# Kernel tuning notes

Hardware: AMD Instinct MI355X
Metric: run time of the kernel (lower is better)

The kernel has to match this reference:

```python
import jax, jax.numpy as jnp
import numpy as np

B, S, HID = 4, 1024, 1024
H = 16
D = HID // H  # 64
SPARSITY = 0.9  # keep prob = 0.1


def setup_inputs() -> dict:
    key = jax.random.key(0)
    ks = jax.random.split(key, 11)
    sc = 1.0 / np.sqrt(HID)
    x = jax.random.normal(ks[0], (B, S, HID), dtype=jnp.float32)
    Wq = jax.random.normal(ks[1], (HID, HID), dtype=jnp.float32) * sc
    bq = jnp.zeros((HID,), dtype=jnp.float32)
    Wk = jax.random.normal(ks[2], (HID, HID), dtype=jnp.float32) * sc
    bk = jnp.zeros((HID,), dtype=jnp.float32)
    Wv = jax.random.normal(ks[3], (HID, HID), dtype=jnp.float32) * sc
    bv = jnp.zeros((HID,), dtype=jnp.float32)
    Wo = jax.random.normal(ks[4], (HID, HID), dtype=jnp.float32) * sc
    bo = jnp.zeros((HID,), dtype=jnp.float32)
    temperature = jnp.ones((H, 1, 1), dtype=jnp.float32)
    # training-mode random sparsity mask: rand > sparsity -> keep (True)
    sparse_mask = jax.random.uniform(ks[5], (B, H, S, S)) > SPARSITY
    return {"x": x, "Wq": Wq, "bq": bq, "Wk": Wk, "bk": bk, "Wv": Wv,
            "bv": bv, "Wo": Wo, "bo": bo, "temperature": temperature,
            "sparse_mask": sparse_mask}


def reference(x, Wq, bq, Wk, bk, Wv, bv, Wo, bo, temperature, sparse_mask):
    b, s, _ = x.shape
    def split_heads(t):
        return t.reshape(b, s, H, D).transpose(0, 2, 1, 3)  # [B,H,S,D]
    q = split_heads(x @ Wq + bq)
    k = split_heads(x @ Wk + bk)
    v = split_heads(x @ Wv + bv)
    scores = jnp.einsum('bhqd,bhkd->bhqk', q, k) / np.sqrt(D)
    scores = scores * temperature  # [H,1,1] broadcasts over [B,H,S,S]
    scores = jnp.where(sparse_mask, scores, -jnp.inf)
    attn = jax.nn.softmax(scores, axis=-1)
    out = jnp.einsum('bhqk,bhkd->bhqd', attn, v)
    out = out.transpose(0, 2, 1, 3).reshape(b, s, HID)
    return out @ Wo + bo
```

## Files before the change

### kernel.cpp

```cpp
#include <hip/hip_runtime.h>

typedef unsigned short u16;
typedef short short8 __attribute__((ext_vector_type(8)));
typedef float f32x4 __attribute__((ext_vector_type(4)));
typedef float float4v __attribute__((ext_vector_type(4)));
typedef u16 u16x4 __attribute__((ext_vector_type(4)));
typedef unsigned long long u64;

__device__ __forceinline__ u16 f2bf(float f) {
  union { float f; unsigned u; } v; v.f = f;
  unsigned r = v.u + 0x7FFFu + ((v.u >> 16) & 1u);
  return (u16)(r >> 16);
}

__device__ __forceinline__ unsigned cvtpk(float lo, float hi) {
  unsigned r;
  asm("v_cvt_pk_bf16_f32 %0, %1, %2" : "=v"(r) : "v"(lo), "v"(hi));
  return r;
}

__device__ __forceinline__ void gload16(const u16* g, u16* l) {
  __builtin_amdgcn_global_load_lds(
      (const __attribute__((address_space(1))) void*)g,
      (__attribute__((address_space(3))) void*)l, 16, 0, 0);
}

__global__ __launch_bounds__(256)
void maskbits_kernel(const void* __restrict__ mask, u64* __restrict__ bits) {
  __shared__ int sf;
  if (threadIdx.x == 0) sf = 0;
  __syncthreads();
  {
    uint4 v = ((const uint4*)mask)[threadIdx.x];
    unsigned xs[4] = {v.x, v.y, v.z, v.w};
    int f = 0;
#pragma unroll
    for (int d = 0; d < 4; ++d) {
      unsigned u = xs[d];
      if (u == 0x3F800000u) f |= 1;
      if (u & 0xFFFFFF00u) f |= 2;
      if ((d & 1) && u) f |= 4;
    }
    if (f) atomicOr(&sf, f);
  }
  __syncthreads();
  const int fl = sf;
  const int fmt = (fl & 1) ? 2 : ((fl & 2) ? 0 : ((fl & 4) ? 1 : 3));

  const int wi = blockIdx.x * 256 + threadIdx.x;
  u64 b = 0;
  if (fmt == 0) {
    const uint4* mp = (const uint4*)mask + (size_t)wi * 4;
#pragma unroll
    for (int i = 0; i < 4; ++i) {
      uint4 v = mp[i];
      unsigned x[4] = {v.x, v.y, v.z, v.w};
#pragma unroll
      for (int d = 0; d < 4; ++d)
#pragma unroll
        for (int by = 0; by < 4; ++by)
          if (x[d] & (0xFFu << (by * 8))) b |= 1ULL << (i * 16 + d * 4 + by);
    }
  } else if (fmt != 3) {
    const uint4* mp = (const uint4*)mask + (size_t)wi * 16;
#pragma unroll
    for (int i = 0; i < 16; ++i) {
      uint4 v = mp[i];
      if (v.x) b |= 1ULL << (i * 4 + 0);
      if (v.y) b |= 1ULL << (i * 4 + 1);
      if (v.z) b |= 1ULL << (i * 4 + 2);
      if (v.w) b |= 1ULL << (i * 4 + 3);
    }
  } else {
    const uint4* mp = (const uint4*)mask + (size_t)wi * 32;
#pragma unroll
    for (int i = 0; i < 32; ++i) {
      uint4 v = mp[i];
      if (v.x | v.y) b |= 1ULL << (i * 2 + 0);
      if (v.z | v.w) b |= 1ULL << (i * 2 + 1);
    }
  }
  int bh = wi >> 14, q = (wi >> 4) & 1023, kt = wi & 15;
  bits[((size_t)bh * 16 + kt) * 1024 + q] = b;
}

__global__ __launch_bounds__(256) void xcvt_kernel(const float* __restrict__ x, u16* __restrict__ xb) {
  int i = (blockIdx.x * 256 + threadIdx.x) * 4;
  float4v v = *(const float4v*)(x + i);
  u16x4 o;
  o[0] = f2bf(v[0]); o[1] = f2bf(v[1]); o[2] = f2bf(v[2]); o[3] = f2bf(v[3]);
  *(u16x4*)(xb + i) = o;
}

__global__ __launch_bounds__(256) void wcvt_kernel(
    const float* __restrict__ W0, const float* __restrict__ W1,
    const float* __restrict__ W2, const float* __restrict__ W3,
    u16* __restrict__ Wt) {
  __shared__ float t[32][33];
  int z = blockIdx.z;
  const float* W = (z == 0) ? W0 : (z == 1) ? W1 : (z == 2) ? W2 : W3;
  u16* out = Wt + (size_t)z * 1024 * 1024;
  int n0 = blockIdx.x * 32, k0 = blockIdx.y * 32;
  int tx = threadIdx.x & 31, ty = threadIdx.x >> 5;
#pragma unroll
  for (int j = 0; j < 4; ++j)
    t[ty + 8 * j][tx] = W[(size_t)(k0 + ty + 8 * j) * 1024 + n0 + tx];
  __syncthreads();
#pragma unroll
  for (int j = 0; j < 4; ++j)
    out[(size_t)(n0 + ty + 8 * j) * 1024 + k0 + tx] = f2bf(t[tx][ty + 8 * j]);
}

__global__ __launch_bounds__(256)
void gemm128_kernel(const u16* __restrict__ A,
                    const u16* __restrict__ BtQ, const u16* __restrict__ BtK, const u16* __restrict__ BtV,
                    const float* __restrict__ bQ, const float* __restrict__ bK, const float* __restrict__ bV,
                    const float* __restrict__ temp,
                    u16* __restrict__ qb, u16* __restrict__ kb, u16* __restrict__ vT,
                    float* __restrict__ fo, int phase) {
  constexpr int K = 1024;
  __shared__ u16 As[128 * 32];
  __shared__ u16 Bs[128 * 32];
  const int tid = threadIdx.x;
  const int lane = tid & 63, w = tid >> 6;
  const int l15 = lane & 15, l4 = lane >> 4;
  const int m0 = blockIdx.x * 128, n0 = blockIdx.y * 128;
  const int z = blockIdx.z;
  const u16* Bt = (z == 0) ? BtQ : (z == 1) ? BtK : BtV;
  const float* bias = (z == 0) ? bQ : (z == 1) ? bK : bV;
  const int wr = w >> 1, wc = w & 1;

  f32x4 acc[4][4] = {};

  const int c0 = tid, c1 = 256 + tid;
  const u16* ga0 = A + (size_t)(m0 + (c0 >> 2)) * K + (c0 & 3) * 8;
  const u16* ga1 = A + (size_t)(m0 + (c1 >> 2)) * K + (c1 & 3) * 8;
  const u16* gb0 = Bt + (size_t)(n0 + (c0 >> 2)) * K + (c0 & 3) * 8;
  const u16* gb1 = Bt + (size_t)(n0 + (c1 >> 2)) * K + (c1 & 3) * 8;
  u16* la0 = As + c0 * 8;
  u16* la1 = As + c1 * 8;
  u16* lb0 = Bs + c0 * 8;
  u16* lb1 = Bs + c1 * 8;

  for (int kt = 0; kt < K; kt += 32) {
    gload16(ga0 + kt, la0);
    gload16(ga1 + kt, la1);
    gload16(gb0 + kt, lb0);
    gload16(gb1 + kt, lb1);
    __syncthreads();
    short8 af[4], bfr[4];
#pragma unroll
    for (int r = 0; r < 4; ++r)
      af[r] = *(const short8*)(As + (wr * 64 + r * 16 + l15) * 32 + l4 * 8);
#pragma unroll
    for (int c = 0; c < 4; ++c)
      bfr[c] = *(const short8*)(Bs + (wc * 64 + c * 16 + l15) * 32 + l4 * 8);
#pragma unroll
    for (int r = 0; r < 4; ++r)
#pragma unroll
      for (int c = 0; c < 4; ++c)
        acc[r][c] = __builtin_amdgcn_mfma_f32_16x16x32_bf16(af[r], bfr[c], acc[r][c], 0, 0, 0);
    __syncthreads();
  }

  float bv4[4], fac4[4];
#pragma unroll
  for (int c = 0; c < 4; ++c) {
    int col = n0 + wc * 64 + c * 16 + l15;
    bv4[c] = bias[col];
    fac4[c] = (phase == 0 && z == 0) ? temp[col >> 6] * 0.18033688011112042f : 1.0f;
  }

#pragma unroll
  for (int r = 0; r < 4; ++r) {
#pragma unroll
    for (int c = 0; c < 4; ++c) {
#pragma unroll
      for (int j = 0; j < 4; ++j) {
        float val = (acc[r][c][j] + bv4[c]) * fac4[c];
        int row = m0 + wr * 64 + r * 16 + l4 * 4 + j;
        int col = n0 + wc * 64 + c * 16 + l15;
        if (phase == 0) {
          int b = row >> 10, s = row & 1023, hh = col >> 6, d = col & 63;
          if (z < 2) {
            u16* dst = (z == 0) ? qb : kb;
            dst[(((size_t)b * 16 + hh) * 1024 + s) * 64 + d] = f2bf(val);
          } else {
            vT[(((size_t)b * 16 + hh) * 64 + d) * 1024 + s] = f2bf(val);
          }
        } else {
          fo[(size_t)row * 1024 + col] = val;
        }
      }
    }
  }
}

__device__ __forceinline__ void softmax_pwrite(const f32x4* s, u64 wcur,
                                               float& m, float& l, f32x4* oacc,
                                               char* Prow, int swzP, int l4) {
  float xx[4][4];
#pragma unroll
  for (int cb = 0; cb < 4; ++cb) {
    unsigned nib = (unsigned)(wcur >> (cb * 16 + l4 * 4)) & 15u;
#pragma unroll
    for (int j = 0; j < 4; ++j)
      xx[cb][j] = ((nib >> j) & 1) ? s[cb][j] : -1e30f;
  }
  float mt = xx[0][0];
#pragma unroll
  for (int cb = 0; cb < 4; ++cb)
#pragma unroll
    for (int j = 0; j < 4; ++j) mt = fmaxf(mt, xx[cb][j]);
  mt = fmaxf(mt, __shfl_xor(mt, 16));
  mt = fmaxf(mt, __shfl_xor(mt, 32));
  if (!__all(mt <= m + 8.f)) {
    float mnew = fmaxf(m, mt);
    float al = exp2f(m - mnew);
    l *= al;
#pragma unroll
    for (int db = 0; db < 4; ++db) oacc[db] *= al;
    m = mnew;
  }
  float rs = 0.f;
#pragma unroll
  for (int cb = 0; cb < 4; ++cb)
#pragma unroll
    for (int j = 0; j < 4; ++j) {
      xx[cb][j] = exp2f(xx[cb][j] - m);
      rs += xx[cb][j];
    }
  rs += __shfl_xor(rs, 16);
  rs += __shfl_xor(rs, 32);
  l += rs;
#pragma unroll
  for (int cb = 0; cb < 4; ++cb) {
    unsigned w0 = cvtpk(xx[cb][0], xx[cb][1]);
    unsigned w1 = cvtpk(xx[cb][2], xx[cb][3]);
    unsigned o2[2] = {w0, w1};
    *(unsigned long long*)(Prow + ((cb * 32 + l4 * 8) ^ swzP)) = *(unsigned long long*)o2;
  }
}

__global__ __launch_bounds__(256)
void attn_kernel(const u16* __restrict__ qb, const u16* __restrict__ kb, const u16* __restrict__ vT,
                 const u64* __restrict__ mbits, u16* __restrict__ oh) {
  __shared__ u16 Ks[2][64 * 64];
  __shared__ u16 Vs[2][64 * 64];
  __shared__ u16 P[4][32 * 64];
  const int tid = threadIdx.x, lane = tid & 63, w = tid >> 6;
  const int l15 = lane & 15, l4 = lane >> 4;
  const int id = blockIdx.x;
  const int xcd = id & 7, sl = id >> 3;
  const int bh = xcd * 8 + (sl >> 3), qx = sl & 7;
  const int b = bh >> 4, h = bh & 15;
  const int q0 = qx * 128 + w * 32;
  const u16* qp = qb + ((size_t)bh * 1024 + q0) * 64;
  const u16* kp = kb + (size_t)bh * 1024 * 64;
  const u16* vp = vT + (size_t)bh * 64 * 1024;
  char* Pw = (char*)&P[w][0];
  const int swzP = (l15 & 7) << 4;
  char* ProwA = Pw + l15 * 128;
  char* ProwB = Pw + (16 + l15) * 128;

  const int L0 = tid, L1 = tid + 256;
  const int r0 = L0 >> 3, cc0 = (L0 & 7) ^ (r0 & 7);
  const int r1 = L1 >> 3, cc1 = (L1 & 7) ^ (r1 & 7);
  const int swzK = (l15 & 7) << 3;

  short8 qa0 = *(const short8*)(qp + (size_t)l15 * 64 + l4 * 8);
  short8 qa1 = *(const short8*)(qp + (size_t)l15 * 64 + 32 + l4 * 8);
  short8 qb0 = *(const short8*)(qp + (size_t)(16 + l15) * 64 + l4 * 8);
  short8 qb1 = *(const short8*)(qp + (size_t)(16 + l15) * 64 + 32 + l4 * 8);

  float ma = -1e30f, la = 0.f, mb_ = -1e30f, lb = 0.f;
  f32x4 oa[4] = {}, ob[4] = {};

  const u64* mba = mbits + (size_t)bh * 16 * 1024 + q0 + l15;
  u64 wa = mba[0], wb = mba[16];

  gload16(kp + (size_t)r0 * 64 + cc0 * 8, &Ks[0][L0 * 8]);
  gload16(kp + (size_t)r1 * 64 + cc1 * 8, &Ks[0][L1 * 8]);
  gload16(vp + (size_t)r0 * 1024 + cc0 * 8, &Vs[0][L0 * 8]);
  gload16(vp + (size_t)r1 * 1024 + cc1 * 8, &Vs[0][L1 * 8]);

  for (int t = 0; t < 16; ++t) {
    const int buf = t & 1;
    __syncthreads();

    if (t < 15) {
      const int k1 = (t + 1) * 64;
      gload16(kp + (size_t)(k1 + r0) * 64 + cc0 * 8, &Ks[buf ^ 1][L0 * 8]);
      gload16(kp + (size_t)(k1 + r1) * 64 + cc1 * 8, &Ks[buf ^ 1][L1 * 8]);
      gload16(vp + (size_t)r0 * 1024 + k1 + cc0 * 8, &Vs[buf ^ 1][L0 * 8]);
      gload16(vp + (size_t)r1 * 1024 + k1 + cc1 * 8, &Vs[buf ^ 1][L1 * 8]);
    }
    u64 wan = 0, wbn = 0;
    if (t < 15) { wan = mba[(t + 1) * 1024]; wbn = mba[(t + 1) * 1024 + 16]; }

    f32x4 sa[4] = {}, sb[4] = {};
    __builtin_amdgcn_s_setprio(1);
#pragma unroll
    for (int cb = 0; cb < 4; ++cb) {
      const u16* kr = &Ks[buf][(cb * 16 + l15) * 64];
      short8 kf0 = *(const short8*)(kr + ((l4 * 8) ^ swzK));
      short8 kf1 = *(const short8*)(kr + ((32 + l4 * 8) ^ swzK));
      sa[cb] = __builtin_amdgcn_mfma_f32_16x16x32_bf16(kf0, qa0, sa[cb], 0, 0, 0);
      sa[cb] = __builtin_amdgcn_mfma_f32_16x16x32_bf16(kf1, qa1, sa[cb], 0, 0, 0);
      sb[cb] = __builtin_amdgcn_mfma_f32_16x16x32_bf16(kf0, qb0, sb[cb], 0, 0, 0);
      sb[cb] = __builtin_amdgcn_mfma_f32_16x16x32_bf16(kf1, qb1, sb[cb], 0, 0, 0);
    }
    __builtin_amdgcn_s_setprio(0);

    softmax_pwrite(sa, wa, ma, la, oa, ProwA, swzP, l4);
    softmax_pwrite(sb, wb, mb_, lb, ob, ProwB, swzP, l4);

    __builtin_amdgcn_s_setprio(1);
#pragma unroll
    for (int ks = 0; ks < 2; ++ks) {
      short8 pa = *(const short8*)(ProwA + ((ks * 64 + l4 * 16) ^ swzP));
      short8 pb = *(const short8*)(ProwB + ((ks * 64 + l4 * 16) ^ swzP));
#pragma unroll
      for (int db = 0; db < 4; ++db) {
        short8 vf = *(const short8*)(&Vs[buf][(db * 16 + l15) * 64 + ((ks * 32 + l4 * 8) ^ swzK)]);
        oa[db] = __builtin_amdgcn_mfma_f32_16x16x32_bf16(vf, pa, oa[db], 0, 0, 0);
        ob[db] = __builtin_amdgcn_mfma_f32_16x16x32_bf16(vf, pb, ob[db], 0, 0, 0);
      }
    }
    __builtin_amdgcn_s_setprio(0);
    wa = wan; wb = wbn;
  }

  float rla = 1.f / la, rlb = 1.f / lb;
  u16* orowA = oh + ((size_t)b * 1024 + q0 + l15) * 1024 + h * 64;
  u16* orowB = oh + ((size_t)b * 1024 + q0 + 16 + l15) * 1024 + h * 64;
#pragma unroll
  for (int db = 0; db < 4; ++db) {
    unsigned a0 = cvtpk(oa[db][0] * rla, oa[db][1] * rla);
    unsigned a1 = cvtpk(oa[db][2] * rla, oa[db][3] * rla);
    unsigned b0 = cvtpk(ob[db][0] * rlb, ob[db][1] * rlb);
    unsigned b1 = cvtpk(ob[db][2] * rlb, ob[db][3] * rlb);
    unsigned oA[2] = {a0, a1}, oB[2] = {b0, b1};
    *(unsigned long long*)(orowA + db * 16 + l4 * 4) = *(unsigned long long*)oA;
    *(unsigned long long*)(orowB + db * 16 + l4 * 4) = *(unsigned long long*)oB;
  }
}

extern "C" void kernel_launch(void* const* d_in, const int* in_sizes, int n_in,
                              void* d_out, int out_size, void* d_ws, size_t ws_size,
                              hipStream_t stream) {
  const float* x = (const float*)d_in[0];
  const float* Wq = (const float*)d_in[1];
  const float* bq = (const float*)d_in[2];
  const float* Wk = (const float*)d_in[3];
  const float* bk = (const float*)d_in[4];
  const float* Wv = (const float*)d_in[5];
  const float* bv = (const float*)d_in[6];
  const float* Wo = (const float*)d_in[7];
  const float* bo = (const float*)d_in[8];
  const float* temp = (const float*)d_in[9];
  const void* mask = (const void*)d_in[10];

  char* ws = (char*)d_ws;
  u16* xb = (u16*)(ws + 256);
  u16* Wt = xb + (size_t)4 * 1024 * 1024;
  u16* qbuf = Wt + (size_t)4 * 1024 * 1024;
  u16* kbuf = qbuf + (size_t)4 * 1024 * 1024;
  u16* vTb = kbuf + (size_t)4 * 1024 * 1024;
  u64* mbits = (u64*)(vTb + (size_t)4 * 1024 * 1024);
  u16* oh = xb;

  maskbits_kernel<<<4096, 256, 0, stream>>>(mask, mbits);
  xcvt_kernel<<<4096, 256, 0, stream>>>(x, xb);
  wcvt_kernel<<<dim3(32, 32, 4), 256, 0, stream>>>(Wq, Wk, Wv, Wo, Wt);
  gemm128_kernel<<<dim3(32, 8, 3), 256, 0, stream>>>(
      xb, Wt, Wt + 1024 * 1024, Wt + 2 * 1024 * 1024,
      bq, bk, bv, temp, qbuf, kbuf, vTb, nullptr, 0);
  attn_kernel<<<512, 256, 0, stream>>>(qbuf, kbuf, vTb, mbits, oh);
  gemm128_kernel<<<dim3(32, 8, 1), 256, 0, stream>>>(
      oh, Wt + 3 * 1024 * 1024, nullptr, nullptr,
      bo, nullptr, nullptr, temp, nullptr, nullptr, nullptr, (float*)d_out, 1);
}
```

Before: 193.1 us.

## Merge prep kernels, transpose V epilogue, widen attention KV tiles, narrow output GEMM

Merges the three preprocessing kernels (mask bit-packing, x conversion, weight transpose/convert) into one launch selected by block index. The V projection now swaps MFMA operands so the transposed V store is contiguous along the sequence. The attention loop loads 128 keys per stage, halving the number of barriers and iterations. The output GEMM uses a 64-wide N tile so it launches twice as many blocks. Together these aim to cut launch overhead, scattered stores and sync cost, at the price of more LDS per attention block and possibly lower occupancy.

```diff
diff --git a/kernel.cpp b/kernel.cpp
--- a/kernel.cpp
+++ b/kernel.cpp
@@ -26,111 +26,116 @@
 }
 
 __global__ __launch_bounds__(256)
-void maskbits_kernel(const void* __restrict__ mask, u64* __restrict__ bits) {
+void prep_kernel(const void* __restrict__ mask, u64* __restrict__ bits,
+                 const float* __restrict__ x, u16* __restrict__ xb,
+                 const float* __restrict__ W0, const float* __restrict__ W1,
+                 const float* __restrict__ W2, const float* __restrict__ W3,
+                 u16* __restrict__ Wt) {
+  __shared__ float t[32][33];
   __shared__ int sf;
-  if (threadIdx.x == 0) sf = 0;
-  __syncthreads();
-  {
-    uint4 v = ((const uint4*)mask)[threadIdx.x];
-    unsigned xs[4] = {v.x, v.y, v.z, v.w};
-    int f = 0;
-#pragma unroll
-    for (int d = 0; d < 4; ++d) {
-      unsigned u = xs[d];
-      if (u == 0x3F800000u) f |= 1;
-      if (u & 0xFFFFFF00u) f |= 2;
-      if ((d & 1) && u) f |= 4;
-    }
-    if (f) atomicOr(&sf, f);
-  }
-  __syncthreads();
-  const int fl = sf;
-  const int fmt = (fl & 1) ? 2 : ((fl & 2) ? 0 : ((fl & 4) ? 1 : 3));
-
-  const int wi = blockIdx.x * 256 + threadIdx.x;
-  u64 b = 0;
-  if (fmt == 0) {
-    const uint4* mp = (const uint4*)mask + (size_t)wi * 4;
-#pragma unroll
-    for (int i = 0; i < 4; ++i) {
-      uint4 v = mp[i];
-      unsigned x[4] = {v.x, v.y, v.z, v.w};
-#pragma unroll
-      for (int d = 0; d < 4; ++d)
-#pragma unroll
-        for (int by = 0; by < 4; ++by)
-          if (x[d] & (0xFFu << (by * 8))) b |= 1ULL << (i * 16 + d * 4 + by);
-    }
-  } else if (fmt != 3) {
-    const uint4* mp = (const uint4*)mask + (size_t)wi * 16;
-#pragma unroll
-    for (int i = 0; i < 16; ++i) {
-      uint4 v = mp[i];
-      if (v.x) b |= 1ULL << (i * 4 + 0);
-      if (v.y) b |= 1ULL << (i * 4 + 1);
-      if (v.z) b |= 1ULL << (i * 4 + 2);
-      if (v.w) b |= 1ULL << (i * 4 + 3);
-    }
+  const int bid = blockIdx.x;
+  if (bid < 4096) {
+    if (threadIdx.x == 0) sf = 0;
+    __syncthreads();
+    {
+      uint4 v = ((const uint4*)mask)[threadIdx.x];
+      unsigned xs[4] = {v.x, v.y, v.z, v.w};
+      int f = 0;
+#pragma unroll
+      for (int d = 0; d < 4; ++d) {
+        unsigned u = xs[d];
+        if (u == 0x3F800000u) f |= 1;
+        if (u & 0xFFFFFF00u) f |= 2;
+        if ((d & 1) && u) f |= 4;
+      }
+      if (f) atomicOr(&sf, f);
+    }
+    __syncthreads();
+    const int fl = sf;
+    const int fmt = (fl & 1) ? 2 : ((fl & 2) ? 0 : ((fl & 4) ? 1 : 3));
+
+    const int wi = bid * 256 + threadIdx.x;
+    u64 b = 0;
+    if (fmt == 0) {
+      const uint4* mp = (const uint4*)mask + (size_t)wi * 4;
+#pragma unroll
+      for (int i = 0; i < 4; ++i) {
+        uint4 v = mp[i];
+        unsigned xw[4] = {v.x, v.y, v.z, v.w};
+#pragma unroll
+        for (int d = 0; d < 4; ++d)
+#pragma unroll
+          for (int by = 0; by < 4; ++by)
+            if (xw[d] & (0xFFu << (by * 8))) b |= 1ULL << (i * 16 + d * 4 + by);
+      }
+    } else if (fmt != 3) {
+      const uint4* mp = (const uint4*)mask + (size_t)wi * 16;
+#pragma unroll
+      for (int i = 0; i < 16; ++i) {
+        uint4 v = mp[i];
+        if (v.x) b |= 1ULL << (i * 4 + 0);
+        if (v.y) b |= 1ULL << (i * 4 + 1);
+        if (v.z) b |= 1ULL << (i * 4 + 2);
+        if (v.w) b |= 1ULL << (i * 4 + 3);
+      }
+    } else {
+      const uint4* mp = (const uint4*)mask + (size_t)wi * 32;
+#pragma unroll
+      for (int i = 0; i < 32; ++i) {
+        uint4 v = mp[i];
+        if (v.x | v.y) b |= 1ULL << (i * 2 + 0);
+        if (v.z | v.w) b |= 1ULL << (i * 2 + 1);
+      }
+    }
+    int bh = wi >> 14, q = (wi >> 4) & 1023, kt = wi & 15;
+    bits[((size_t)bh * 16 + kt) * 1024 + q] = b;
+  } else if (bid < 8192) {
+    int i = ((bid - 4096) * 256 + threadIdx.x) * 4;
+    float4v v = *(const float4v*)(x + i);
+    u16x4 o;
+    o[0] = f2bf(v[0]); o[1] = f2bf(v[1]); o[2] = f2bf(v[2]); o[3] = f2bf(v[3]);
+    *(u16x4*)(xb + i) = o;
   } else {
-    const uint4* mp = (const uint4*)mask + (size_t)wi * 32;
-#pragma unroll
-    for (int i = 0; i < 32; ++i) {
-      uint4 v = mp[i];
-      if (v.x | v.y) b |= 1ULL << (i * 2 + 0);
-      if (v.z | v.w) b |= 1ULL << (i * 2 + 1);
-    }
-  }
-  int bh = wi >> 14, q = (wi >> 4) & 1023, kt = wi & 15;
-  bits[((size_t)bh * 16 + kt) * 1024 + q] = b;
-}
-
-__global__ __launch_bounds__(256) void xcvt_kernel(const float* __restrict__ x, u16* __restrict__ xb) {
-  int i = (blockIdx.x * 256 + threadIdx.x) * 4;
-  float4v v = *(const float4v*)(x + i);
-  u16x4 o;
-  o[0] = f2bf(v[0]); o[1] = f2bf(v[1]); o[2] = f2bf(v[2]); o[3] = f2bf(v[3]);
-  *(u16x4*)(xb + i) = o;
-}
-
-__global__ __launch_bounds__(256) void wcvt_kernel(
-    const float* __restrict__ W0, const float* __restrict__ W1,
-    const float* __restrict__ W2, const float* __restrict__ W3,
-    u16* __restrict__ Wt) {
-  __shared__ float t[32][33];
-  int z = blockIdx.z;
-  const float* W = (z == 0) ? W0 : (z == 1) ? W1 : (z == 2) ? W2 : W3;
-  u16* out = Wt + (size_t)z * 1024 * 1024;
-  int n0 = blockIdx.x * 32, k0 = blockIdx.y * 32;
-  int tx = threadIdx.x & 31, ty = threadIdx.x >> 5;
-#pragma unroll
-  for (int j = 0; j < 4; ++j)
-    t[ty + 8 * j][tx] = W[(size_t)(k0 + ty + 8 * j) * 1024 + n0 + tx];
-  __syncthreads();
-#pragma unroll
-  for (int j = 0; j < 4; ++j)
-    out[(size_t)(n0 + ty + 8 * j) * 1024 + k0 + tx] = f2bf(t[tx][ty + 8 * j]);
-}
-
+    int i = bid - 8192;
+    int z = i >> 10, rest = i & 1023;
+    const float* W = (z == 0) ? W0 : (z == 1) ? W1 : (z == 2) ? W2 : W3;
+    u16* out = Wt + (size_t)z * 1024 * 1024;
+    int n0 = (rest & 31) * 32, k0 = (rest >> 5) * 32;
+    int tx = threadIdx.x & 31, ty = threadIdx.x >> 5;
+#pragma unroll
+    for (int j = 0; j < 4; ++j)
+      t[ty + 8 * j][tx] = W[(size_t)(k0 + ty + 8 * j) * 1024 + n0 + tx];
+    __syncthreads();
+#pragma unroll
+    for (int j = 0; j < 4; ++j)
+      out[(size_t)(n0 + ty + 8 * j) * 1024 + k0 + tx] = f2bf(t[tx][ty + 8 * j]);
+  }
+}
+
+template<int BN>
 __global__ __launch_bounds__(256)
-void gemm128_kernel(const u16* __restrict__ A,
-                    const u16* __restrict__ BtQ, const u16* __restrict__ BtK, const u16* __restrict__ BtV,
-                    const float* __restrict__ bQ, const float* __restrict__ bK, const float* __restrict__ bV,
-                    const float* __restrict__ temp,
-                    u16* __restrict__ qb, u16* __restrict__ kb, u16* __restrict__ vT,
-                    float* __restrict__ fo, int phase) {
+void gemm_kernel(const u16* __restrict__ A,
+                 const u16* __restrict__ Bt0, const u16* __restrict__ Bt1, const u16* __restrict__ Bt2,
+                 const float* __restrict__ b0, const float* __restrict__ b1, const float* __restrict__ b2,
+                 const float* __restrict__ temp,
+                 u16* __restrict__ qb, u16* __restrict__ kb, u16* __restrict__ vT,
+                 float* __restrict__ fo, int phase) {
   constexpr int K = 1024;
+  constexpr int WN = BN / 2;
+  constexpr int NC = WN / 16;
   __shared__ u16 As[128 * 32];
-  __shared__ u16 Bs[128 * 32];
+  __shared__ u16 Bs[BN * 32];
   const int tid = threadIdx.x;
   const int lane = tid & 63, w = tid >> 6;
   const int l15 = lane & 15, l4 = lane >> 4;
-  const int m0 = blockIdx.x * 128, n0 = blockIdx.y * 128;
+  const int m0 = blockIdx.x * 128, n0 = blockIdx.y * BN;
   const int z = blockIdx.z;
-  const u16* Bt = (z == 0) ? BtQ : (z == 1) ? BtK : BtV;
-  const float* bias = (z == 0) ? bQ : (z == 1) ? bK : bV;
+  const u16* Bt = (z == 0) ? Bt0 : (z == 1) ? Bt1 : Bt2;
+  const float* bias = (z == 0) ? b0 : (z == 1) ? b1 : b2;
   const int wr = w >> 1, wc = w & 1;
-
-  f32x4 acc[4][4] = {};
+  const bool ct = (phase == 0) && (z == 2);
+
+  f32x4 acc[4][NC] = {};
 
   const int c0 = tid, c1 = 256 + tid;
   const u16* ga0 = A + (size_t)(m0 + (c0 >> 2)) * K + (c0 & 3) * 8;
@@ -146,50 +151,76 @@
     gload16(ga0 + kt, la0);
     gload16(ga1 + kt, la1);
     gload16(gb0 + kt, lb0);
-    gload16(gb1 + kt, lb1);
-    __syncthreads();
-    short8 af[4], bfr[4];
+    if (BN == 128) gload16(gb1 + kt, lb1);
+    __syncthreads();
+    short8 af[4], bfr[NC];
 #pragma unroll
     for (int r = 0; r < 4; ++r)
       af[r] = *(const short8*)(As + (wr * 64 + r * 16 + l15) * 32 + l4 * 8);
 #pragma unroll
-    for (int c = 0; c < 4; ++c)
-      bfr[c] = *(const short8*)(Bs + (wc * 64 + c * 16 + l15) * 32 + l4 * 8);
-#pragma unroll
-    for (int r = 0; r < 4; ++r)
-#pragma unroll
-      for (int c = 0; c < 4; ++c)
-        acc[r][c] = __builtin_amdgcn_mfma_f32_16x16x32_bf16(af[r], bfr[c], acc[r][c], 0, 0, 0);
-    __syncthreads();
-  }
-
-  float bv4[4], fac4[4];
-#pragma unroll
-  for (int c = 0; c < 4; ++c) {
-    int col = n0 + wc * 64 + c * 16 + l15;
-    bv4[c] = bias[col];
-    fac4[c] = (phase == 0 && z == 0) ? temp[col >> 6] * 0.18033688011112042f : 1.0f;
-  }
-
-#pragma unroll
-  for (int r = 0; r < 4; ++r) {
-#pragma unroll
-    for (int c = 0; c < 4; ++c) {
-#pragma unroll
-      for (int j = 0; j < 4; ++j) {
-        float val = (acc[r][c][j] + bv4[c]) * fac4[c];
-        int row = m0 + wr * 64 + r * 16 + l4 * 4 + j;
-        int col = n0 + wc * 64 + c * 16 + l15;
-        if (phase == 0) {
-          int b = row >> 10, s = row & 1023, hh = col >> 6, d = col & 63;
-          if (z < 2) {
+    for (int c = 0; c < NC; ++c)
+      bfr[c] = *(const short8*)(Bs + (wc * WN + c * 16 + l15) * 32 + l4 * 8);
+    if (ct) {
+#pragma unroll
+      for (int r = 0; r < 4; ++r)
+#pragma unroll
+        for (int c = 0; c < NC; ++c)
+          acc[r][c] = __builtin_amdgcn_mfma_f32_16x16x32_bf16(bfr[c], af[r], acc[r][c], 0, 0, 0);
+    } else {
+#pragma unroll
+      for (int r = 0; r < 4; ++r)
+#pragma unroll
+        for (int c = 0; c < NC; ++c)
+          acc[r][c] = __builtin_amdgcn_mfma_f32_16x16x32_bf16(af[r], bfr[c], acc[r][c], 0, 0, 0);
+    }
+    __syncthreads();
+  }
+
+  if (ct) {
+    float bvj[NC][4];
+#pragma unroll
+    for (int c = 0; c < NC; ++c)
+#pragma unroll
+      for (int j = 0; j < 4; ++j)
+        bvj[c][j] = bias[n0 + wc * WN + c * 16 + l4 * 4 + j];
+#pragma unroll
+    for (int r = 0; r < 4; ++r) {
+#pragma unroll
+      for (int c = 0; c < NC; ++c) {
+#pragma unroll
+        for (int j = 0; j < 4; ++j) {
+          float val = acc[r][c][j] + bvj[c][j];
+          int n = n0 + wc * WN + c * 16 + l4 * 4 + j;
+          int mm = m0 + wr * 64 + r * 16 + l15;
+          int b = mm >> 10, s = mm & 1023;
+          vT[((size_t)b * 1024 + n) * 1024 + s] = f2bf(val);
+        }
+      }
+    }
+  } else {
+    float bv4[NC], fac4[NC];
+#pragma unroll
+    for (int c = 0; c < NC; ++c) {
+      int col = n0 + wc * WN + c * 16 + l15;
+      bv4[c] = bias[col];
+      fac4[c] = (phase == 0 && z == 0) ? temp[col >> 6] * 0.18033688011112042f : 1.0f;
+    }
+#pragma unroll
+    for (int r = 0; r < 4; ++r) {
+#pragma unroll
+      for (int c = 0; c < NC; ++c) {
+#pragma unroll
+        for (int j = 0; j < 4; ++j) {
+          float val = (acc[r][c][j] + bv4[c]) * fac4[c];
+          int row = m0 + wr * 64 + r * 16 + l4 * 4 + j;
+          int col = n0 + wc * WN + c * 16 + l15;
+          if (phase == 0) {
+            int b = row >> 10, s = row & 1023, hh = col >> 6, d = col & 63;
             u16* dst = (z == 0) ? qb : kb;
             dst[(((size_t)b * 16 + hh) * 1024 + s) * 64 + d] = f2bf(val);
           } else {
-            vT[(((size_t)b * 16 + hh) * 64 + d) * 1024 + s] = f2bf(val);
+            fo[(size_t)row * 1024 + col] = val;
           }
-        } else {
-          fo[(size_t)row * 1024 + col] = val;
         }
       }
     }
@@ -245,8 +276,8 @@
 __global__ __launch_bounds__(256)
 void attn_kernel(const u16* __restrict__ qb, const u16* __restrict__ kb, const u16* __restrict__ vT,
                  const u64* __restrict__ mbits, u16* __restrict__ oh) {
-  __shared__ u16 Ks[2][64 * 64];
-  __shared__ u16 Vs[2][64 * 64];
+  __shared__ u16 Ks[2][128 * 64];
+  __shared__ u16 Vs[2][64 * 128];
   __shared__ u16 P[4][32 * 64];
   const int tid = threadIdx.x, lane = tid & 63, w = tid >> 6;
   const int l15 = lane & 15, l4 = lane >> 4;
@@ -262,73 +293,88 @@
   const int swzP = (l15 & 7) << 4;
   char* ProwA = Pw + l15 * 128;
   char* ProwB = Pw + (16 + l15) * 128;
-
-  const int L0 = tid, L1 = tid + 256;
-  const int r0 = L0 >> 3, cc0 = (L0 & 7) ^ (r0 & 7);
-  const int r1 = L1 >> 3, cc1 = (L1 & 7) ^ (r1 & 7);
   const int swzK = (l15 & 7) << 3;
+
+  int krow[4], kcol[4], vrow[4], vcol[4];
+#pragma unroll
+  for (int i = 0; i < 4; ++i) {
+    int c = tid + 256 * i;
+    krow[i] = c >> 3; kcol[i] = ((c & 7) ^ (krow[i] & 7)) * 8;
+    vrow[i] = c >> 4; vcol[i] = ((c & 15) ^ (vrow[i] & 7)) * 8;
+  }
 
   short8 qa0 = *(const short8*)(qp + (size_t)l15 * 64 + l4 * 8);
   short8 qa1 = *(const short8*)(qp + (size_t)l15 * 64 + 32 + l4 * 8);
   short8 qb0 = *(const short8*)(qp + (size_t)(16 + l15) * 64 + l4 * 8);
   short8 qb1 = *(const short8*)(qp + (size_t)(16 + l15) * 64 + 32 + l4 * 8);
 
-  float ma = -1e30f, la = 0.f, mb_ = -1e30f, lb = 0.f;
+  float ma = -1e30f, la = 0.f, mbv = -1e30f, lb = 0.f;
   f32x4 oa[4] = {}, ob[4] = {};
 
   const u64* mba = mbits + (size_t)bh * 16 * 1024 + q0 + l15;
-  u64 wa = mba[0], wb = mba[16];
-
-  gload16(kp + (size_t)r0 * 64 + cc0 * 8, &Ks[0][L0 * 8]);
-  gload16(kp + (size_t)r1 * 64 + cc1 * 8, &Ks[0][L1 * 8]);
-  gload16(vp + (size_t)r0 * 1024 + cc0 * 8, &Vs[0][L0 * 8]);
-  gload16(vp + (size_t)r1 * 1024 + cc1 * 8, &Vs[0][L1 * 8]);
-
-  for (int t = 0; t < 16; ++t) {
+  u64 wa[2], wb[2];
+  wa[0] = mba[0]; wa[1] = mba[1024];
+  wb[0] = mba[16]; wb[1] = mba[1024 + 16];
+
+#pragma unroll
+  for (int i = 0; i < 4; ++i) {
+    gload16(kp + (size_t)krow[i] * 64 + kcol[i], &Ks[0][(tid + 256 * i) * 8]);
+    gload16(vp + (size_t)vrow[i] * 1024 + vcol[i], &Vs[0][(tid + 256 * i) * 8]);
+  }
+
+  for (int t = 0; t < 8; ++t) {
     const int buf = t & 1;
     __syncthreads();
 
-    if (t < 15) {
-      const int k1 = (t + 1) * 64;
-      gload16(kp + (size_t)(k1 + r0) * 64 + cc0 * 8, &Ks[buf ^ 1][L0 * 8]);
-      gload16(kp + (size_t)(k1 + r1) * 64 + cc1 * 8, &Ks[buf ^ 1][L1 * 8]);
-      gload16(vp + (size_t)r0 * 1024 + k1 + cc0 * 8, &Vs[buf ^ 1][L0 * 8]);
-      gload16(vp + (size_t)r1 * 1024 + k1 + cc1 * 8, &Vs[buf ^ 1][L1 * 8]);
-    }
-    u64 wan = 0, wbn = 0;
-    if (t < 15) { wan = mba[(t + 1) * 1024]; wbn = mba[(t + 1) * 1024 + 16]; }
-
-    f32x4 sa[4] = {}, sb[4] = {};
-    __builtin_amdgcn_s_setprio(1);
-#pragma unroll
-    for (int cb = 0; cb < 4; ++cb) {
-      const u16* kr = &Ks[buf][(cb * 16 + l15) * 64];
-      short8 kf0 = *(const short8*)(kr + ((l4 * 8) ^ swzK));
-      short8 kf1 = *(const short8*)(kr + ((32 + l4 * 8) ^ swzK));
-      sa[cb] = __builtin_amdgcn_mfma_f32_16x16x32_bf16(kf0, qa0, sa[cb], 0, 0, 0);
-      sa[cb] = __builtin_amdgcn_mfma_f32_16x16x32_bf16(kf1, qa1, sa[cb], 0, 0, 0);
-      sb[cb] = __builtin_amdgcn_mfma_f32_16x16x32_bf16(kf0, qb0, sb[cb], 0, 0, 0);
-      sb[cb] = __builtin_amdgcn_mfma_f32_16x16x32_bf16(kf1, qb1, sb[cb], 0, 0, 0);
-    }
-    __builtin_amdgcn_s_setprio(0);
-
-    softmax_pwrite(sa, wa, ma, la, oa, ProwA, swzP, l4);
-    softmax_pwrite(sb, wb, mb_, lb, ob, ProwB, swzP, l4);
-
-    __builtin_amdgcn_s_setprio(1);
-#pragma unroll
-    for (int ks = 0; ks < 2; ++ks) {
-      short8 pa = *(const short8*)(ProwA + ((ks * 64 + l4 * 16) ^ swzP));
-      short8 pb = *(const short8*)(ProwB + ((ks * 64 + l4 * 16) ^ swzP));
-#pragma unroll
-      for (int db = 0; db < 4; ++db) {
-        short8 vf = *(const short8*)(&Vs[buf][(db * 16 + l15) * 64 + ((ks * 32 + l4 * 8) ^ swzK)]);
-        oa[db] = __builtin_amdgcn_mfma_f32_16x16x32_bf16(vf, pa, oa[db], 0, 0, 0);
-        ob[db] = __builtin_amdgcn_mfma_f32_16x16x32_bf16(vf, pb, ob[db], 0, 0, 0);
-      }
-    }
-    __builtin_amdgcn_s_setprio(0);
-    wa = wan; wb = wbn;
+    if (t < 7) {
+      const int k1 = (t + 1) * 128;
+#pragma unroll
+      for (int i = 0; i < 4; ++i) {
+        gload16(kp + (size_t)(k1 + krow[i]) * 64 + kcol[i], &Ks[buf ^ 1][(tid + 256 * i) * 8]);
+        gload16(vp + (size_t)vrow[i] * 1024 + k1 + vcol[i], &Vs[buf ^ 1][(tid + 256 * i) * 8]);
+      }
+    }
+    u64 nwa[2] = {0, 0}, nwb[2] = {0, 0};
+    if (t < 7) {
+      nwa[0] = mba[(2 * t + 2) * 1024];      nwa[1] = mba[(2 * t + 3) * 1024];
+      nwb[0] = mba[(2 * t + 2) * 1024 + 16]; nwb[1] = mba[(2 * t + 3) * 1024 + 16];
+    }
+
+#pragma unroll
+    for (int st = 0; st < 2; ++st) {
+      f32x4 sa[4] = {}, sb[4] = {};
+      __builtin_amdgcn_s_setprio(1);
+#pragma unroll
+      for (int cb = 0; cb < 4; ++cb) {
+        const u16* kr = &Ks[buf][(st * 64 + cb * 16 + l15) * 64];
+        short8 kf0 = *(const short8*)(kr + ((l4 * 8) ^ swzK));
+        short8 kf1 = *(const short8*)(kr + ((32 + l4 * 8) ^ swzK));
+        sa[cb] = __builtin_amdgcn_mfma_f32_16x16x32_bf16(kf0, qa0, sa[cb], 0, 0, 0);
+        sa[cb] = __builtin_amdgcn_mfma_f32_16x16x32_bf16(kf1, qa1, sa[cb], 0, 0, 0);
+        sb[cb] = __builtin_amdgcn_mfma_f32_16x16x32_bf16(kf0, qb0, sb[cb], 0, 0, 0);
+        sb[cb] = __builtin_amdgcn_mfma_f32_16x16x32_bf16(kf1, qb1, sb[cb], 0, 0, 0);
+      }
+      __builtin_amdgcn_s_setprio(0);
+
+      softmax_pwrite(sa, wa[st], ma, la, oa, ProwA, swzP, l4);
+      softmax_pwrite(sb, wb[st], mbv, lb, ob, ProwB, swzP, l4);
+
+      __builtin_amdgcn_s_setprio(1);
+#pragma unroll
+      for (int ks = 0; ks < 2; ++ks) {
+        short8 pa = *(const short8*)(ProwA + ((ks * 64 + l4 * 16) ^ swzP));
+        short8 pbf = *(const short8*)(ProwB + ((ks * 64 + l4 * 16) ^ swzP));
+#pragma unroll
+        for (int db = 0; db < 4; ++db) {
+          short8 vf = *(const short8*)(&Vs[buf][(db * 16 + l15) * 128 +
+                                                ((st * 64 + ks * 32 + l4 * 8) ^ swzK)]);
+          oa[db] = __builtin_amdgcn_mfma_f32_16x16x32_bf16(vf, pa, oa[db], 0, 0, 0);
+          ob[db] = __builtin_amdgcn_mfma_f32_16x16x32_bf16(vf, pbf, ob[db], 0, 0, 0);
+        }
+      }
+      __builtin_amdgcn_s_setprio(0);
+    }
+    wa[0] = nwa[0]; wa[1] = nwa[1]; wb[0] = nwb[0]; wb[1] = nwb[1];
   }
 
   float rla = 1.f / la, rlb = 1.f / lb;
@@ -370,14 +416,12 @@
   u64* mbits = (u64*)(vTb + (size_t)4 * 1024 * 1024);
   u16* oh = xb;
 
-  maskbits_kernel<<<4096, 256, 0, stream>>>(mask, mbits);
-  xcvt_kernel<<<4096, 256, 0, stream>>>(x, xb);
-  wcvt_kernel<<<dim3(32, 32, 4), 256, 0, stream>>>(Wq, Wk, Wv, Wo, Wt);
-  gemm128_kernel<<<dim3(32, 8, 3), 256, 0, stream>>>(
+  prep_kernel<<<12288, 256, 0, stream>>>(mask, mbits, x, xb, Wq, Wk, Wv, Wo, Wt);
+  gemm_kernel<128><<<dim3(32, 8, 3), 256, 0, stream>>>(
       xb, Wt, Wt + 1024 * 1024, Wt + 2 * 1024 * 1024,
       bq, bk, bv, temp, qbuf, kbuf, vTb, nullptr, 0);
   attn_kernel<<<512, 256, 0, stream>>>(qbuf, kbuf, vTb, mbits, oh);
-  gemm128_kernel<<<dim3(32, 8, 1), 256, 0, stream>>>(
+  gemm_kernel<64><<<dim3(32, 16, 1), 256, 0, stream>>>(
       oh, Wt + 3 * 1024 * 1024, nullptr, nullptr,
       bo, nullptr, nullptr, temp, nullptr, nullptr, nullptr, (float*)d_out, 1);
 }
```

Result: no change. 192.1 us (-0.5%).
